# Kernel optimization log

Measured on AMD Instinct MI355X. Metric: run time of the kernel, lower is better.

Reference implementation:

```python
import jax, jax.numpy as jnp
import numpy as np

SIZE = 512
ATTN = 64      # per-head attention_size
OUT = 64       # per-head output_size
HEADS = 8

def setup_inputs() -> dict:
    key = jax.random.key(0)
    ks = jax.random.split(key, 7)
    s = 0.02
    return {
        "x":  jax.random.normal(ks[0], (4, 2048, SIZE), dtype=jnp.float32),
        "Wq": jax.random.normal(ks[1], (SIZE, ATTN * HEADS), dtype=jnp.float32) * s,
        "bq": jax.random.normal(ks[2], (ATTN * HEADS,), dtype=jnp.float32) * s,
        "Wk": jax.random.normal(ks[3], (SIZE, ATTN), dtype=jnp.float32) * s,  # shared key, no bias
        "Wv": jax.random.normal(ks[4], (SIZE, OUT * HEADS), dtype=jnp.float32) * s,
        "bv": jax.random.normal(ks[5], (OUT * HEADS,), dtype=jnp.float32) * s,
    }

def reference(x, Wq, bq, Wk, Wv, bv):
    B, S, _ = x.shape
    q = (x @ Wq + bq).reshape(B, S, HEADS, ATTN)   # (B,S,H,A)
    k = x @ Wk                                      # (B,S,A) shared across heads
    v = (x @ Wv + bv).reshape(B, S, HEADS, OUT)     # (B,S,H,O)
    # NOTE: original divides by sqrt(seq_len), not sqrt(head_dim)
    scale = 1.0 / np.sqrt(S).astype(np.float32)
    scores = jnp.einsum("bqha,bka->bhqk", q, k) * scale  # (B,H,S,S)
    causal = jnp.tril(jnp.ones((S, S), dtype=bool))
    scores = jnp.where(causal, scores, -jnp.inf)
    attn = jax.nn.softmax(scores, axis=-1)
    out = jnp.einsum("bhqk,bkho->bqho", attn, v)    # (B,S,H,O)
    return out.reshape(B, S, HEADS * OUT)
```

## Files before the change

kernel.cpp:

```cpp
#include <hip/hip_runtime.h>
#include <math.h>


typedef _Float16 half8 __attribute__((ext_vector_type(8)));
typedef _Float16 half4 __attribute__((ext_vector_type(4)));
typedef float float4v __attribute__((ext_vector_type(4)));
typedef unsigned int u32;

#define SCL2E 0.031885926f

__device__ inline float4v mfma16(half8 a, half8 b, float4v c) {
    return __builtin_amdgcn_mfma_f32_16x16x32_f16(a, b, c, 0, 0, 0);
}
__device__ inline void load16(const _Float16* g, _Float16* l) {
    __builtin_amdgcn_global_load_lds((const __attribute__((address_space(1))) u32*)g,
                                     (__attribute__((address_space(3))) u32*)l, 16, 0, 0);
}

__global__ __launch_bounds__(256) void prep(
    const float* __restrict__ x, const float* __restrict__ Wq,
    const float* __restrict__ Wk, const float* __restrict__ Wv,
    _Float16* __restrict__ xh, _Float16* __restrict__ wqt,
    _Float16* __restrict__ wkt, _Float16* __restrict__ wvt) {
    const int bid = blockIdx.x;
    if (bid < 2048) {
        size_t base = (size_t)bid * 2048 + (size_t)threadIdx.x * 8;
        const float4* xp = (const float4*)(x + base);
        float4 f0 = xp[0], f1 = xp[1];
        half8 h = {(_Float16)f0.x, (_Float16)f0.y, (_Float16)f0.z, (_Float16)f0.w,
                   (_Float16)f1.x, (_Float16)f1.y, (_Float16)f1.z, (_Float16)f1.w};
        *(half8*)(xh + base) = h;
    } else {
        int r = bid - 2048;
        const float* W; _Float16* WT; int N, bx, by;
        if (r < 256)      { W = Wq; WT = wqt; N = 512; bx = r & 15; by = r >> 4; }
        else if (r < 288) { r -= 256; W = Wk; WT = wkt; N = 64;  bx = r & 1;  by = r >> 1; }
        else              { r -= 288; W = Wv; WT = wvt; N = 512; bx = r & 15; by = r >> 4; }
        __shared__ float T[32][33];
        const int tx = threadIdx.x & 31, ty = threadIdx.x >> 5;
        const int n0 = bx * 32, k0 = by * 32;
#pragma unroll
        for (int i = 0; i < 4; ++i)
            T[ty + 8 * i][tx] = W[(size_t)(k0 + ty + 8 * i) * N + n0 + tx];
        __syncthreads();
#pragma unroll
        for (int i = 0; i < 4; ++i)
            WT[(size_t)(n0 + ty + 8 * i) * 512 + k0 + tx] = (_Float16)T[tx][ty + 8 * i];
    }
}

__global__ __launch_bounds__(256) void qkv_gemm(
    const _Float16* __restrict__ xh,
    const _Float16* __restrict__ wqt, const _Float16* __restrict__ wkt,
    const _Float16* __restrict__ wvt,
    const float* __restrict__ bq, const float* __restrict__ bv,
    _Float16* __restrict__ q_ws, _Float16* __restrict__ kt_ws, _Float16* __restrict__ vt_ws) {
    __shared__ __align__(16) _Float16 Xs[2][8192];
    __shared__ __align__(16) _Float16 Ws[2][4096];

    const int m0 = blockIdx.x * 128;
    const int nt = blockIdx.y;
    const _Float16* WT;
    const float* bias;
    if (nt < 8)       { WT = wqt + (size_t)nt * 64 * 512; bias = bq + nt * 64; }
    else if (nt == 8) { WT = wkt;                          bias = nullptr; }
    else              { WT = wvt + (size_t)(nt - 9) * 64 * 512; bias = bv + (nt - 9) * 64; }

    const int tid = threadIdx.x;
    const int w = tid >> 6, lane = tid & 63, quad = lane >> 4, cl = lane & 15;
    const int lrow = lane >> 3;
    const int lgc = (lane & 7) ^ lrow;
    const _Float16* xg = xh + (size_t)(m0 + lrow) * 512 + lgc * 8;
    const _Float16* wg = WT + (size_t)lrow * 512 + lgc * 8;

    const int g0 = (quad ^ (cl & 7)) << 3;
    const int g1 = ((quad ^ 4) ^ (cl & 7)) << 3;

    float4v acc[2][4] = {};

#pragma unroll
    for (int c = 0; c < 4; ++c) {
        int cc = w * 4 + c;
        load16(xg + (size_t)cc * 8 * 512, Xs[0] + cc * 512);
    }
#pragma unroll
    for (int c = 0; c < 2; ++c) {
        int cc = w * 2 + c;
        load16(wg + (size_t)cc * 8 * 512, Ws[0] + cc * 512);
    }

    for (int ki = 0; ki < 8; ++ki) {
        const int cb = ki & 1, nb = cb ^ 1;
        __syncthreads();
        if (ki < 7) {
            const int kk = (ki + 1) * 64;
#pragma unroll
            for (int c = 0; c < 4; ++c) {
                int cc = w * 4 + c;
                load16(xg + (size_t)cc * 8 * 512 + kk, Xs[nb] + cc * 512);
            }
#pragma unroll
            for (int c = 0; c < 2; ++c) {
                int cc = w * 2 + c;
                load16(wg + (size_t)cc * 8 * 512 + kk, Ws[nb] + cc * 512);
            }
        }
#pragma unroll
        for (int c = 0; c < 2; ++c) {
            const int g = c ? g1 : g0;
#pragma unroll
            for (int s = 0; s < 2; ++s) {
                half8 a = *(const half8*)(Xs[cb] + (w * 32 + s * 16 + cl) * 64 + g);
#pragma unroll
                for (int j = 0; j < 4; ++j) {
                    half8 b = *(const half8*)(Ws[cb] + (j * 16 + cl) * 64 + g);
                    acc[s][j] = mfma16(a, b, acc[s][j]);
                }
            }
        }
    }

    if (nt < 8) {
#pragma unroll
        for (int s = 0; s < 2; ++s)
#pragma unroll
            for (int j = 0; j < 4; ++j)
#pragma unroll
                for (int r = 0; r < 4; ++r) {
                    int lr = w * 32 + s * 16 + quad * 4 + r;
                    int col = j * 16 + cl;
                    q_ws[(size_t)(m0 + lr) * 512 + nt * 64 + col] =
                        (_Float16)((acc[s][j][r] + bias[col]) * SCL2E);
                }
    } else if (nt == 8) {
#pragma unroll
        for (int s = 0; s < 2; ++s)
#pragma unroll
            for (int j = 0; j < 4; ++j)
#pragma unroll
                for (int r = 0; r < 4; ++r) {
                    int grow = m0 + w * 32 + s * 16 + quad * 4 + r;
                    int b = grow >> 11, t = (grow >> 6) & 31, row = grow & 63;
                    int col = j * 16 + cl;
                    kt_ws[((size_t)(b * 32 + t) << 12) + row * 64 +
                          (((col >> 3) ^ (row & 7)) << 3) + (col & 7)] = (_Float16)acc[s][j][r];
                }
    } else {
        const int h = nt - 9;
#pragma unroll
        for (int s = 0; s < 2; ++s)
#pragma unroll
            for (int j = 0; j < 4; ++j)
#pragma unroll
                for (int r = 0; r < 4; ++r) {
                    int grow = m0 + w * 32 + s * 16 + quad * 4 + r;
                    int b = grow >> 11, t = (grow >> 6) & 31, row = grow & 63;
                    int o = j * 16 + cl;
                    int kap = ((row & 15) << 2) + (row >> 4);
                    vt_ws[(((size_t)(b * 8 + h) * 32 + t) << 12) + o * 64 +
                          (((kap >> 3) ^ (o & 7)) << 3) + (kap & 7)] =
                        (_Float16)(acc[s][j][r] + bias[o]);
                }
    }
}

__global__ __launch_bounds__(256, 4) void attn(
    const _Float16* __restrict__ q_ws, const _Float16* __restrict__ kt_ws,
    const _Float16* __restrict__ vt_ws, float* __restrict__ out) {
    __shared__ __align__(16) _Float16 Ks[2][4096];
    __shared__ __align__(16) _Float16 VTs[2][4096];
    __shared__ __align__(16) _Float16 Ps[4][1024];

    const int bh = blockIdx.x, b = bh >> 3, h = bh & 7;
    const int y = blockIdx.y;
    int qt, half;
    if (y < 8)       { qt = 15 - y; half = 1; }
    else if (y < 16) { qt = y - 8;  half = 1; }
    else if (y < 24) { qt = 31 - y; half = 0; }
    else             { qt = y - 24; half = 0; }
    const int tlast = 2 * qt + half;
    const int q0 = qt * 128 + half * 64;

    const int bS = b * 2048;
    const int tid = threadIdx.x;
    const int w = tid >> 6, lane = tid & 63, quad = lane >> 4, cl = lane & 15;

    const _Float16* kbase = kt_ws + ((size_t)(b * 32) << 12);
    const _Float16* vbase = vt_ws + ((size_t)((b * 8 + h) * 32) << 12);

    const int g0 = (quad ^ (cl & 7)) << 3;
    const int g1 = ((quad ^ 4) ^ (cl & 7)) << 3;
    const int so0 = w * 1024 + lane * 8;

    const _Float16* qbase = q_ws + (size_t)(bS + q0 + w * 16 + cl) * 512 + h * 64;
    half8 qa0 = *(const half8*)(qbase + quad * 8);
    half8 qa1 = *(const half8*)(qbase + 32 + quad * 8);

    float4v oacc[4] = {};
    float l_run[4] = {0.f, 0.f, 0.f, 0.f};

    load16(kbase + so0,       &Ks[0][w * 1024]);
    load16(kbase + so0 + 512, &Ks[0][w * 1024 + 512]);
    load16(vbase + so0,       &VTs[0][w * 1024]);
    load16(vbase + so0 + 512, &VTs[0][w * 1024 + 512]);

    for (int t = 0; t <= tlast; ++t) {
        const int cb = t & 1, nb = cb ^ 1;
        __syncthreads();
        if (t < tlast) {
            const _Float16* kt = kbase + ((size_t)(t + 1) << 12);
            const _Float16* vt = vbase + ((size_t)(t + 1) << 12);
            load16(kt + so0,       &Ks[nb][w * 1024]);
            load16(kt + so0 + 512, &Ks[nb][w * 1024 + 512]);
            load16(vt + so0,       &VTs[nb][w * 1024]);
            load16(vt + so0 + 512, &VTs[nb][w * 1024 + 512]);
        }
        const int ww = (t == tlast) ? w : 100;
        const int jmax = ww < 3 ? ww : 3;
        float4v sfr[4];
#pragma unroll
        for (int j = 0; j < 4; ++j) {
            if (j <= jmax) {
                const _Float16* kr = &Ks[cb][(j * 16 + cl) * 64];
                half8 b0 = *(const half8*)(kr + g0);
                half8 b1 = *(const half8*)(kr + g1);
                float4v a_ = {0.f, 0.f, 0.f, 0.f};
                a_ = mfma16(qa0, b0, a_);
                a_ = mfma16(qa1, b1, a_);
                sfr[j] = a_;
            }
        }
#pragma unroll
        for (int r = 0; r < 4; ++r) {
            float pj[4];
#pragma unroll
            for (int j = 0; j < 4; ++j) {
                bool live = (j < jmax) || (j == jmax && (ww > 3 || cl <= quad * 4 + r));
                pj[j] = live ? exp2f(sfr[j][r]) : 0.f;
            }
            l_run[r] += (pj[0] + pj[1]) + (pj[2] + pj[3]);
            int rr = quad * 4 + r;
            half4 ph = {(_Float16)pj[0], (_Float16)pj[1], (_Float16)pj[2], (_Float16)pj[3]};
            *(half4*)&Ps[w][rr * 64 + ((((cl >> 1) ^ (rr & 7)) << 3) | ((cl & 1) << 2))] = ph;
        }
        const _Float16* PB = &Ps[w][cl * 64];
        half8 pa0 = *(const half8*)(PB + g0);
        half8 pa1 = *(const half8*)(PB + g1);
#pragma unroll
        for (int jo = 0; jo < 4; ++jo) {
            const _Float16* vr = &VTs[cb][(jo * 16 + cl) * 64];
            half8 v0 = *(const half8*)(vr + g0);
            half8 v1 = *(const half8*)(vr + g1);
            oacc[jo] = mfma16(pa0, v0, oacc[jo]);
            oacc[jo] = mfma16(pa1, v1, oacc[jo]);
        }
    }
#pragma unroll
    for (int r = 0; r < 4; ++r) {
        float l = l_run[r];
        l += __shfl_xor(l, 1);
        l += __shfl_xor(l, 2);
        l += __shfl_xor(l, 4);
        l += __shfl_xor(l, 8);
        float inv = 1.0f / l;
        int row = q0 + w * 16 + quad * 4 + r;
        float* op = out + (size_t)(bS + row) * 512 + h * 64 + cl;
        op[0]  = oacc[0][r] * inv;
        op[16] = oacc[1][r] * inv;
        op[32] = oacc[2][r] * inv;
        op[48] = oacc[3][r] * inv;
    }
}

extern "C" void kernel_launch(void* const* d_in, const int* in_sizes, int n_in,
                              void* d_out, int out_size, void* d_ws, size_t ws_size,
                              hipStream_t stream) {
    const float* x  = (const float*)d_in[0];
    const float* Wq = (const float*)d_in[1];
    const float* bq = (const float*)d_in[2];
    const float* Wk = (const float*)d_in[3];
    const float* Wv = (const float*)d_in[4];
    const float* bv = (const float*)d_in[5];
    float* out = (float*)d_out;

    char* ws = (char*)d_ws;
    _Float16* q_ws  = (_Float16*)(ws);
    _Float16* kt_ws = (_Float16*)(ws + 8388608);
    _Float16* vt_ws = (_Float16*)(ws + 9437184);
    _Float16* wqt   = (_Float16*)(ws + 17825792);
    _Float16* wkt   = (_Float16*)(ws + 18350080);
    _Float16* wvt   = (_Float16*)(ws + 18415616);
    _Float16* xh    = (_Float16*)(ws + 18939904);

    prep<<<dim3(2592), dim3(256), 0, stream>>>(x, Wq, Wk, Wv, xh, wqt, wkt, wvt);

    qkv_gemm<<<dim3(64, 17), dim3(256), 0, stream>>>(
        xh, wqt, wkt, wvt, bq, bv, q_ws, kt_ws, vt_ws);

    attn<<<dim3(32, 32), dim3(256), 0, stream>>>(q_ws, kt_ws, vt_ws, out);
}
```

Measured before the change: 144.5 us.

## Split attention KV range across two wave groups per block with LDS reduction

The attention kernel now launches 512 threads per block. Two groups of four waves each process half of the causal key tiles for the same 64-row query tile, and their partial outputs and row sums are combined through shared memory at the end. This is a split-K style scheme meant to shorten the serial loop for long causal rows and cut the load imbalance across blocks. A specialised unmasked path is also added for non-diagonal tiles. The cost is twice the LDS for K/V buffers, an extra reduction pass with two barriers, and fewer blocks resident per CU.

```diff
diff --git a/kernel.cpp b/kernel.cpp
--- a/kernel.cpp
+++ b/kernel.cpp
@@ -164,111 +164,159 @@
     }
 }
 
-__global__ __launch_bounds__(256, 4) void attn(
+__global__ __launch_bounds__(512, 2) void attn(
     const _Float16* __restrict__ q_ws, const _Float16* __restrict__ kt_ws,
     const _Float16* __restrict__ vt_ws, float* __restrict__ out) {
-    __shared__ __align__(16) _Float16 Ks[2][4096];
-    __shared__ __align__(16) _Float16 VTs[2][4096];
-    __shared__ __align__(16) _Float16 Ps[4][1024];
+    __shared__ __align__(16) _Float16 Ks[2][2][4096];
+    __shared__ __align__(16) _Float16 VTs[2][2][4096];
+    __shared__ __align__(16) _Float16 Ps[8][1024];
 
     const int bh = blockIdx.x, b = bh >> 3, h = bh & 7;
-    const int y = blockIdx.y;
-    int qt, half;
-    if (y < 8)       { qt = 15 - y; half = 1; }
-    else if (y < 16) { qt = y - 8;  half = 1; }
-    else if (y < 24) { qt = 31 - y; half = 0; }
-    else             { qt = y - 24; half = 0; }
-    const int tlast = 2 * qt + half;
-    const int q0 = qt * 128 + half * 64;
+    const int p = 31 - blockIdx.y;
+    const int q0 = p * 64;
+    const int nmax = (p + 2) >> 1;
 
     const int bS = b * 2048;
     const int tid = threadIdx.x;
     const int w = tid >> 6, lane = tid & 63, quad = lane >> 4, cl = lane & 15;
+    const int g = w >> 2, wl = w & 3;
+    const int tbase = g ? nmax : 0;
+    const int nit = g ? (p + 1 - nmax) : nmax;
 
     const _Float16* kbase = kt_ws + ((size_t)(b * 32) << 12);
     const _Float16* vbase = vt_ws + ((size_t)((b * 8 + h) * 32) << 12);
 
     const int g0 = (quad ^ (cl & 7)) << 3;
     const int g1 = ((quad ^ 4) ^ (cl & 7)) << 3;
-    const int so0 = w * 1024 + lane * 8;
-
-    const _Float16* qbase = q_ws + (size_t)(bS + q0 + w * 16 + cl) * 512 + h * 64;
+    const int so0 = wl * 1024 + lane * 8;
+
+    const _Float16* qbase = q_ws + (size_t)(bS + q0 + wl * 16 + cl) * 512 + h * 64;
     half8 qa0 = *(const half8*)(qbase + quad * 8);
     half8 qa1 = *(const half8*)(qbase + 32 + quad * 8);
 
     float4v oacc[4] = {};
     float l_run[4] = {0.f, 0.f, 0.f, 0.f};
 
-    load16(kbase + so0,       &Ks[0][w * 1024]);
-    load16(kbase + so0 + 512, &Ks[0][w * 1024 + 512]);
-    load16(vbase + so0,       &VTs[0][w * 1024]);
-    load16(vbase + so0 + 512, &VTs[0][w * 1024 + 512]);
-
-    for (int t = 0; t <= tlast; ++t) {
+    if (nit > 0) {
+        const _Float16* kt = kbase + ((size_t)tbase << 12);
+        const _Float16* vt = vbase + ((size_t)tbase << 12);
+        load16(kt + so0,       &Ks[g][0][wl * 1024]);
+        load16(kt + so0 + 512, &Ks[g][0][wl * 1024 + 512]);
+        load16(vt + so0,       &VTs[g][0][wl * 1024]);
+        load16(vt + so0 + 512, &VTs[g][0][wl * 1024 + 512]);
+    }
+
+    for (int t = 0; t < nmax; ++t) {
         const int cb = t & 1, nb = cb ^ 1;
         __syncthreads();
-        if (t < tlast) {
-            const _Float16* kt = kbase + ((size_t)(t + 1) << 12);
-            const _Float16* vt = vbase + ((size_t)(t + 1) << 12);
-            load16(kt + so0,       &Ks[nb][w * 1024]);
-            load16(kt + so0 + 512, &Ks[nb][w * 1024 + 512]);
-            load16(vt + so0,       &VTs[nb][w * 1024]);
-            load16(vt + so0 + 512, &VTs[nb][w * 1024 + 512]);
-        }
-        const int ww = (t == tlast) ? w : 100;
-        const int jmax = ww < 3 ? ww : 3;
-        float4v sfr[4];
-#pragma unroll
-        for (int j = 0; j < 4; ++j) {
-            if (j <= jmax) {
-                const _Float16* kr = &Ks[cb][(j * 16 + cl) * 64];
-                half8 b0 = *(const half8*)(kr + g0);
-                half8 b1 = *(const half8*)(kr + g1);
-                float4v a_ = {0.f, 0.f, 0.f, 0.f};
-                a_ = mfma16(qa0, b0, a_);
-                a_ = mfma16(qa1, b1, a_);
-                sfr[j] = a_;
-            }
-        }
+        const int tg = tbase + t;
+        if (t + 1 < nit) {
+            const _Float16* kt = kbase + ((size_t)(tg + 1) << 12);
+            const _Float16* vt = vbase + ((size_t)(tg + 1) << 12);
+            load16(kt + so0,       &Ks[g][nb][wl * 1024]);
+            load16(kt + so0 + 512, &Ks[g][nb][wl * 1024 + 512]);
+            load16(vt + so0,       &VTs[g][nb][wl * 1024]);
+            load16(vt + so0 + 512, &VTs[g][nb][wl * 1024 + 512]);
+        }
+        if (t < nit) {
+            if (tg != p) {
+                float4v sfr[4];
+#pragma unroll
+                for (int j = 0; j < 4; ++j) {
+                    const _Float16* kr = &Ks[g][cb][(j * 16 + cl) * 64];
+                    half8 b0 = *(const half8*)(kr + g0);
+                    half8 b1 = *(const half8*)(kr + g1);
+                    float4v a_ = {0.f, 0.f, 0.f, 0.f};
+                    a_ = mfma16(qa0, b0, a_);
+                    a_ = mfma16(qa1, b1, a_);
+                    sfr[j] = a_;
+                }
+#pragma unroll
+                for (int r = 0; r < 4; ++r) {
+                    float p0 = exp2f(sfr[0][r]), p1 = exp2f(sfr[1][r]);
+                    float p2 = exp2f(sfr[2][r]), p3 = exp2f(sfr[3][r]);
+                    l_run[r] += (p0 + p1) + (p2 + p3);
+                    int rr = quad * 4 + r;
+                    half4 ph = {(_Float16)p0, (_Float16)p1, (_Float16)p2, (_Float16)p3};
+                    *(half4*)&Ps[w][rr * 64 + ((((cl >> 1) ^ (rr & 7)) << 3) | ((cl & 1) << 2))] = ph;
+                }
+            } else {
+                const int jmax = wl;
+                float4v sfr[4];
+#pragma unroll
+                for (int j = 0; j < 4; ++j) {
+                    if (j <= jmax) {
+                        const _Float16* kr = &Ks[g][cb][(j * 16 + cl) * 64];
+                        half8 b0 = *(const half8*)(kr + g0);
+                        half8 b1 = *(const half8*)(kr + g1);
+                        float4v a_ = {0.f, 0.f, 0.f, 0.f};
+                        a_ = mfma16(qa0, b0, a_);
+                        a_ = mfma16(qa1, b1, a_);
+                        sfr[j] = a_;
+                    }
+                }
+#pragma unroll
+                for (int r = 0; r < 4; ++r) {
+                    float pj[4];
+#pragma unroll
+                    for (int j = 0; j < 4; ++j) {
+                        bool live = (j < jmax) || (j == jmax && cl <= quad * 4 + r);
+                        pj[j] = live ? exp2f(sfr[j][r]) : 0.f;
+                    }
+                    l_run[r] += (pj[0] + pj[1]) + (pj[2] + pj[3]);
+                    int rr = quad * 4 + r;
+                    half4 ph = {(_Float16)pj[0], (_Float16)pj[1], (_Float16)pj[2], (_Float16)pj[3]};
+                    *(half4*)&Ps[w][rr * 64 + ((((cl >> 1) ^ (rr & 7)) << 3) | ((cl & 1) << 2))] = ph;
+                }
+            }
+            const _Float16* PB = &Ps[w][cl * 64];
+            half8 pa0 = *(const half8*)(PB + g0);
+            half8 pa1 = *(const half8*)(PB + g1);
+#pragma unroll
+            for (int jo = 0; jo < 4; ++jo) {
+                const _Float16* vr = &VTs[g][cb][(jo * 16 + cl) * 64];
+                half8 v0 = *(const half8*)(vr + g0);
+                half8 v1 = *(const half8*)(vr + g1);
+                oacc[jo] = mfma16(pa0, v0, oacc[jo]);
+                oacc[jo] = mfma16(pa1, v1, oacc[jo]);
+            }
+        }
+    }
+
+    __syncthreads();
+    float* Obuf = (float*)&Ks[1][0][0];
+    float* Lbuf = (float*)&Ps[4][0];
+    if (g == 1) {
+#pragma unroll
+        for (int jo = 0; jo < 4; ++jo)
+#pragma unroll
+            for (int r = 0; r < 4; ++r) {
+                int row = wl * 16 + quad * 4 + r;
+                Obuf[row * 64 + jo * 16 + cl] = oacc[jo][r];
+            }
 #pragma unroll
         for (int r = 0; r < 4; ++r) {
-            float pj[4];
-#pragma unroll
-            for (int j = 0; j < 4; ++j) {
-                bool live = (j < jmax) || (j == jmax && (ww > 3 || cl <= quad * 4 + r));
-                pj[j] = live ? exp2f(sfr[j][r]) : 0.f;
-            }
-            l_run[r] += (pj[0] + pj[1]) + (pj[2] + pj[3]);
-            int rr = quad * 4 + r;
-            half4 ph = {(_Float16)pj[0], (_Float16)pj[1], (_Float16)pj[2], (_Float16)pj[3]};
-            *(half4*)&Ps[w][rr * 64 + ((((cl >> 1) ^ (rr & 7)) << 3) | ((cl & 1) << 2))] = ph;
-        }
-        const _Float16* PB = &Ps[w][cl * 64];
-        half8 pa0 = *(const half8*)(PB + g0);
-        half8 pa1 = *(const half8*)(PB + g1);
-#pragma unroll
-        for (int jo = 0; jo < 4; ++jo) {
-            const _Float16* vr = &VTs[cb][(jo * 16 + cl) * 64];
-            half8 v0 = *(const half8*)(vr + g0);
-            half8 v1 = *(const half8*)(vr + g1);
-            oacc[jo] = mfma16(pa0, v0, oacc[jo]);
-            oacc[jo] = mfma16(pa1, v1, oacc[jo]);
-        }
-    }
-#pragma unroll
-    for (int r = 0; r < 4; ++r) {
-        float l = l_run[r];
-        l += __shfl_xor(l, 1);
-        l += __shfl_xor(l, 2);
-        l += __shfl_xor(l, 4);
-        l += __shfl_xor(l, 8);
-        float inv = 1.0f / l;
-        int row = q0 + w * 16 + quad * 4 + r;
-        float* op = out + (size_t)(bS + row) * 512 + h * 64 + cl;
-        op[0]  = oacc[0][r] * inv;
-        op[16] = oacc[1][r] * inv;
-        op[32] = oacc[2][r] * inv;
-        op[48] = oacc[3][r] * inv;
+            int row = wl * 16 + quad * 4 + r;
+            Lbuf[row * 16 + cl] = l_run[r];
+        }
+    }
+    __syncthreads();
+    if (g == 0) {
+#pragma unroll
+        for (int r = 0; r < 4; ++r) {
+            int row = wl * 16 + quad * 4 + r;
+            float l = l_run[r] + Lbuf[row * 16 + cl];
+            l += __shfl_xor(l, 1);
+            l += __shfl_xor(l, 2);
+            l += __shfl_xor(l, 4);
+            l += __shfl_xor(l, 8);
+            float inv = 1.0f / l;
+            float* op = out + (size_t)(bS + q0 + row) * 512 + h * 64 + cl;
+            op[0]  = (oacc[0][r] + Obuf[row * 64 +      cl]) * inv;
+            op[16] = (oacc[1][r] + Obuf[row * 64 + 16 + cl]) * inv;
+            op[32] = (oacc[2][r] + Obuf[row * 64 + 32 + cl]) * inv;
+            op[48] = (oacc[3][r] + Obuf[row * 64 + 48 + cl]) * inv;
+        }
     }
 }
 
@@ -297,5 +345,5 @@
     qkv_gemm<<<dim3(64, 17), dim3(256), 0, stream>>>(
         xh, wqt, wkt, wvt, bq, bv, q_ws, kt_ws, vt_ws);
 
-    attn<<<dim3(32, 32), dim3(256), 0, stream>>>(q_ws, kt_ws, vt_ws, out);
-}
+    attn<<<dim3(32, 32), dim3(512), 0, stream>>>(q_ws, kt_ws, vt_ws, out);
+}
```

New measurement: 142.8 us. No clear change (-1.2%).
